# Kernel tuning notes

Measured on AMD Instinct MI355X. Metric: run time of the kernel, lower is better.

## Reference

```python
import jax, jax.numpy as jnp
import numpy as np


def setup_inputs() -> dict:
    key = jax.random.key(0)
    k1, k2 = jax.random.split(key)
    B, N, M = 8, 8192, 8192
    source_points = jax.random.normal(k1, (B, N, 3), dtype=jnp.float32)
    target_points = jax.random.normal(k2, (B, M, 3), dtype=jnp.float32)
    return {"source_points": source_points, "target_points": target_points}


def reference(source_points, target_points):
    # dist: [B, N, M]  (same math as (x[:, :, None] - y[:, None]) ** 2 summed over coords)
    s_sq = jnp.sum(source_points ** 2, axis=-1)  # [B, N]
    t_sq = jnp.sum(target_points ** 2, axis=-1)  # [B, M]
    cross = jnp.einsum("bnd,bmd->bnm", source_points, target_points)  # [B, N, M]
    dist = s_sq[:, :, None] + t_sq[:, None, :] - 2.0 * cross
    min_s2t = jnp.min(dist, axis=2)  # [B, N] nearest target for each source point
    min_t2s = jnp.min(dist, axis=1)  # [B, M] nearest source for each target point
    chamfer = jnp.mean(min_s2t, axis=1) + jnp.mean(min_t2s, axis=1)  # [B]
    return chamfer
```

## Files before the change

kernel.cpp:

```cpp
#include <hip/hip_runtime.h>


typedef float f32x16 __attribute__((ext_vector_type(16)));
typedef short bf16x8 __attribute__((ext_vector_type(8)));

constexpr int BATCH  = 8;
constexpr int NPTS   = 8192;
constexpr int BLOCK  = 256;
constexpr int QTILE  = 256;
constexpr int QB     = NPTS / QTILE;
constexpr int DSPLIT = 4;
constexpr int DBR    = NPTS / DSPLIT;
constexpr int CH     = 256;
constexpr int NCH    = DBR / CH;

constexpr size_t FRAGB_N = (size_t)BATCH * NPTS * 2;
constexpr size_t SM_N    = (size_t)BATCH * NPTS;

static __device__ __forceinline__ float fmin3(float a, float b, float c) {
    return fminf(fminf(a, b), c);
}
static __device__ __forceinline__ unsigned short bf16h(float f) {
    unsigned int u = __float_as_uint(f);
    u += 0x7fffu + ((u >> 16) & 1u);
    return (unsigned short)(u >> 16);
}
static __device__ __forceinline__ float bf16tof(unsigned short h) {
    return __uint_as_float(((unsigned int)h) << 16);
}
static __device__ __forceinline__ unsigned int pack2(unsigned short a, unsigned short b) {
    return (unsigned int)a | ((unsigned int)b << 16);
}
static __device__ __forceinline__ float tree16(const f32x16& a) {
    float m = fmin3(a[0], a[1], a[2]);
    m = fmin3(m, a[3], a[4]);   m = fmin3(m, a[5], a[6]);
    m = fmin3(m, a[7], a[8]);   m = fmin3(m, a[9], a[10]);
    m = fmin3(m, a[11], a[12]); m = fmin3(m, a[13], a[14]);
    return fminf(m, a[15]);
}

__global__ __launch_bounds__(BLOCK) void chamfer_prep(
    const float* __restrict__ tgt, uint4* __restrict__ fragB,
    unsigned int* __restrict__ smins, unsigned int* __restrict__ tmins,
    float* __restrict__ out)
{
    const int i = blockIdx.x * BLOCK + threadIdx.x;
    const float* tp = tgt + (size_t)i * 3;
    float px = tp[0], py = tp[1], pz = tp[2];
    float nx = -px, ny = -py, nz = -pz;
    float ht = 0.5f * fmaf(px, px, fmaf(py, py, pz * pz));
    const unsigned short one = bf16h(1.0f);
    unsigned short nxh = bf16h(nx), nxl = bf16h(nx - bf16tof(nxh));
    unsigned short nyh = bf16h(ny), nyl = bf16h(ny - bf16tof(nyh));
    unsigned short nzh = bf16h(nz), nzl = bf16h(nz - bf16tof(nzh));
    unsigned short hh = bf16h(ht),  hl = bf16h(ht - bf16tof(hh));
    fragB[2 * i + 0] = make_uint4(pack2(nxh, nxl), pack2(nxh, nyh),
                                  pack2(nyl, nyh), pack2(nzh, nzl));
    fragB[2 * i + 1] = make_uint4(pack2(nzh, one), pack2(one, hh),
                                  pack2(hl, 0), 0u);
    smins[i] = 0x7f7f7f7fu;
    tmins[i] = 0x7f7f7f7fu;
    if (i < BATCH) out[i] = 0.0f;
}

__global__ __launch_bounds__(BLOCK) void chamfer_nn(
    const float* __restrict__ src, const uint4* __restrict__ fragB,
    unsigned int* __restrict__ smins, unsigned int* __restrict__ tmins)
{
    __shared__ uint4 Bfr0[CH], Bfr1[CH];
    __shared__ int   sht[NCH][CH];

    const int tid  = threadIdx.x;
    const int lane = tid & 63;
    const int w    = tid >> 6;
    const int half = lane >> 5;
    const int l31  = lane & 31;
    const int qb   = blockIdx.x;
    const int b    = blockIdx.y;
    const int ds   = blockIdx.z;

#pragma unroll
    for (int c = 0; c < NCH; c++) sht[c][tid] = 0x7f7f7f7f;

    const unsigned short one = bf16h(1.0f);
    bf16x8 af0, af1;
#pragma unroll
    for (int g = 0; g < 2; g++) {
        const int q = qb * QTILE + w * 64 + g * 32 + l31;
        const float* qp = src + ((size_t)b * NPTS + q) * 3;
        float qx = qp[0], qy = qp[1], qz = qp[2];
        float hq = 0.5f * fmaf(qx, qx, fmaf(qy, qy, qz * qz));
        unsigned short xh = bf16h(qx), xl = bf16h(qx - bf16tof(xh));
        unsigned short yh = bf16h(qy), yl = bf16h(qy - bf16tof(yh));
        unsigned short zh = bf16h(qz), zl = bf16h(qz - bf16tof(zh));
        unsigned short qh = bf16h(hq), ql = bf16h(hq - bf16tof(qh));
        bf16x8 a;
        if (half == 0) {
            a[0] = (short)xh; a[1] = (short)xh; a[2] = (short)xl;
            a[3] = (short)yh; a[4] = (short)yh; a[5] = (short)yl;
            a[6] = (short)zh; a[7] = (short)zh;
        } else {
            a[0] = (short)zl; a[1] = (short)qh; a[2] = (short)ql;
            a[3] = (short)one; a[4] = (short)one;
            a[5] = 0; a[6] = 0; a[7] = 0;
        }
        if (g == 0) af0 = a; else af1 = a;
    }

    float rmn0[16], rmn1[16];
#pragma unroll
    for (int r = 0; r < 16; r++) { rmn0[r] = 3.4e38f; rmn1[r] = 3.4e38f; }
    const f32x16 zz = {};
    const uint4* Bh = half ? Bfr1 : Bfr0;

    const uint4* fb = fragB + ((size_t)b * NPTS + (size_t)ds * DBR) * 2;

    uint4 r0 = fb[2 * tid + 0], r1 = fb[2 * tid + 1];

    for (int c = 0; c < NCH; ++c) {
        __syncthreads();
        Bfr0[tid] = r0;
        Bfr1[tid] = r1;
        __syncthreads();
        if (c + 1 < NCH) {
            r0 = fb[2 * ((c + 1) * CH + tid) + 0];
            r1 = fb[2 * ((c + 1) * CH + tid) + 1];
        }

#pragma unroll
        for (int tp = 0; tp < CH / 64; ++tp) {
            const int t0 = tp * 2, t1 = tp * 2 + 1;
            bf16x8 b0 = *reinterpret_cast<const bf16x8*>(&Bh[t0 * 32 + l31]);
            bf16x8 b1 = *reinterpret_cast<const bf16x8*>(&Bh[t1 * 32 + l31]);
            f32x16 a00 = __builtin_amdgcn_mfma_f32_32x32x16_bf16(af0, b0, zz, 0, 0, 0);
            f32x16 a01 = __builtin_amdgcn_mfma_f32_32x32x16_bf16(af0, b1, zz, 0, 0, 0);
            f32x16 a10 = __builtin_amdgcn_mfma_f32_32x32x16_bf16(af1, b0, zz, 0, 0, 0);
            f32x16 a11 = __builtin_amdgcn_mfma_f32_32x32x16_bf16(af1, b1, zz, 0, 0, 0);
#pragma unroll
            for (int r = 0; r < 16; r++) {
                rmn0[r] = fmin3(rmn0[r], a00[r], a01[r]);
                rmn1[r] = fmin3(rmn1[r], a10[r], a11[r]);
            }
            float c0 = fminf(tree16(a00), tree16(a10));
            float c1 = fminf(tree16(a01), tree16(a11));
            atomicMin(&sht[c][t0 * 32 + l31], __float_as_int(c0));
            atomicMin(&sht[c][t1 * 32 + l31], __float_as_int(c1));
        }
    }
    __syncthreads();

    unsigned int* tm = tmins + (size_t)b * NPTS + (size_t)ds * DBR;
#pragma unroll
    for (int c = 0; c < NCH; c++) {
        float v = fmaxf(__int_as_float(sht[c][tid]), 0.0f);
        atomicMin(&tm[c * CH + tid], __float_as_uint(v));
    }

    unsigned int* sm = smins + (size_t)b * NPTS;
    const int qbase = qb * QTILE + w * 64;
#pragma unroll
    for (int r = 0; r < 16; r++) {
        float a = rmn0[r], bv = rmn1[r];
#pragma unroll
        for (int off = 16; off > 0; off >>= 1) {
            a  = fminf(a,  __shfl_xor(a,  off, 64));
            bv = fminf(bv, __shfl_xor(bv, off, 64));
        }
        if (l31 == 0) {
            const int row = (r & 3) + 8 * (r >> 2) + 4 * half;
            atomicMin(&sm[qbase + row],      __float_as_uint(fmaxf(a,  0.0f)));
            atomicMin(&sm[qbase + 32 + row], __float_as_uint(fmaxf(bv, 0.0f)));
        }
    }
}

__global__ __launch_bounds__(BLOCK) void chamfer_final(
    const unsigned int* __restrict__ smins, const unsigned int* __restrict__ tmins,
    float* __restrict__ out)
{
    const int seg = blockIdx.x;
    const int b   = blockIdx.y;
    const int tid = threadIdx.x;
    float acc = 0.0f;
#pragma unroll
    for (int k = 0; k < 8; k++) {
        const size_t i = (size_t)b * NPTS + seg * 2048 + k * BLOCK + tid;
        acc += __uint_as_float(smins[i]) + __uint_as_float(tmins[i]);
    }
    for (int off = 32; off > 0; off >>= 1) acc += __shfl_down(acc, off, 64);
    __shared__ float wsum[4];
    if ((tid & 63) == 0) wsum[tid >> 6] = acc;
    __syncthreads();
    if (tid == 0)
        atomicAdd(&out[b],
                  (wsum[0] + wsum[1] + wsum[2] + wsum[3]) * (2.0f / (float)NPTS));
}

extern "C" void kernel_launch(void* const* d_in, const int* in_sizes, int n_in,
                              void* d_out, int out_size, void* d_ws, size_t ws_size,
                              hipStream_t stream) {
    const float* src = (const float*)d_in[0];
    const float* tgt = (const float*)d_in[1];
    float* out = (float*)d_out;

    uint4* fragB        = (uint4*)d_ws;
    unsigned int* smins = (unsigned int*)(fragB + FRAGB_N);
    unsigned int* tmins = smins + SM_N;

    chamfer_prep<<<BATCH * NPTS / BLOCK, BLOCK, 0, stream>>>(tgt, fragB, smins, tmins, out);
    chamfer_nn<<<dim3(QB, BATCH, DSPLIT), BLOCK, 0, stream>>>(src, fragB, smins, tmins);
    chamfer_final<<<dim3(4, BATCH), BLOCK, 0, stream>>>(smins, tmins, out);
}
```

Before: 106.2 us.

## Compute both NN directions as separate row-min passes instead of column atomics

Drops the per-tile column reduction (tree16 plus LDS atomicMin per MFMA pair) that produced target-to-source minima. It adds a second set of blocks that swap the roles of source and target, so both directions use only the cheap row-min path, and it halves the database split to keep the grid size unchanged. This doubles the MFMA work in exchange for removing the heavy column-reduction ALU and LDS atomic traffic, and the prep kernel now builds fragments for both point sets.

```diff
diff --git a/kernel.cpp b/kernel.cpp
--- a/kernel.cpp
+++ b/kernel.cpp
@@ -9,13 +9,13 @@
 constexpr int BLOCK  = 256;
 constexpr int QTILE  = 256;
 constexpr int QB     = NPTS / QTILE;
-constexpr int DSPLIT = 4;
+constexpr int DSPLIT = 2;
 constexpr int DBR    = NPTS / DSPLIT;
 constexpr int CH     = 256;
 constexpr int NCH    = DBR / CH;
 
-constexpr size_t FRAGB_N = (size_t)BATCH * NPTS * 2;
-constexpr size_t SM_N    = (size_t)BATCH * NPTS;
+constexpr size_t FRAG_N = (size_t)BATCH * NPTS * 2;
+constexpr size_t SM_N   = (size_t)BATCH * NPTS;
 
 static __device__ __forceinline__ float fmin3(float a, float b, float c) {
     return fminf(fminf(a, b), c);
@@ -31,44 +31,48 @@
 static __device__ __forceinline__ unsigned int pack2(unsigned short a, unsigned short b) {
     return (unsigned int)a | ((unsigned int)b << 16);
 }
-static __device__ __forceinline__ float tree16(const f32x16& a) {
-    float m = fmin3(a[0], a[1], a[2]);
-    m = fmin3(m, a[3], a[4]);   m = fmin3(m, a[5], a[6]);
-    m = fmin3(m, a[7], a[8]);   m = fmin3(m, a[9], a[10]);
-    m = fmin3(m, a[11], a[12]); m = fmin3(m, a[13], a[14]);
-    return fminf(m, a[15]);
-}
-
-__global__ __launch_bounds__(BLOCK) void chamfer_prep(
-    const float* __restrict__ tgt, uint4* __restrict__ fragB,
-    unsigned int* __restrict__ smins, unsigned int* __restrict__ tmins,
-    float* __restrict__ out)
-{
-    const int i = blockIdx.x * BLOCK + threadIdx.x;
-    const float* tp = tgt + (size_t)i * 3;
-    float px = tp[0], py = tp[1], pz = tp[2];
+
+static __device__ __forceinline__ void make_bfrag(float px, float py, float pz,
+                                                  uint4& p0, uint4& p1) {
+    const unsigned short one = bf16h(1.0f);
     float nx = -px, ny = -py, nz = -pz;
     float ht = 0.5f * fmaf(px, px, fmaf(py, py, pz * pz));
-    const unsigned short one = bf16h(1.0f);
     unsigned short nxh = bf16h(nx), nxl = bf16h(nx - bf16tof(nxh));
     unsigned short nyh = bf16h(ny), nyl = bf16h(ny - bf16tof(nyh));
     unsigned short nzh = bf16h(nz), nzl = bf16h(nz - bf16tof(nzh));
     unsigned short hh = bf16h(ht),  hl = bf16h(ht - bf16tof(hh));
-    fragB[2 * i + 0] = make_uint4(pack2(nxh, nxl), pack2(nxh, nyh),
-                                  pack2(nyl, nyh), pack2(nzh, nzl));
-    fragB[2 * i + 1] = make_uint4(pack2(nzh, one), pack2(one, hh),
-                                  pack2(hl, 0), 0u);
-    smins[i] = 0x7f7f7f7fu;
-    tmins[i] = 0x7f7f7f7fu;
+    p0 = make_uint4(pack2(nxh, nxl), pack2(nxh, nyh),
+                    pack2(nyl, nyh), pack2(nzh, nzl));
+    p1 = make_uint4(pack2(nzh, one), pack2(one, hh),
+                    pack2(hl, 0), 0u);
+}
+
+__global__ __launch_bounds__(BLOCK) void chamfer_prep(
+    const float* __restrict__ src, const float* __restrict__ tgt,
+    uint4* __restrict__ fragS, uint4* __restrict__ fragT,
+    unsigned int* __restrict__ mins, float* __restrict__ out)
+{
+    const int i = blockIdx.x * BLOCK + threadIdx.x;
+    uint4 p0, p1;
+    const float* tp = tgt + (size_t)i * 3;
+    make_bfrag(tp[0], tp[1], tp[2], p0, p1);
+    fragT[2 * i + 0] = p0;
+    fragT[2 * i + 1] = p1;
+    const float* sp = src + (size_t)i * 3;
+    make_bfrag(sp[0], sp[1], sp[2], p0, p1);
+    fragS[2 * i + 0] = p0;
+    fragS[2 * i + 1] = p1;
+    mins[i]        = 0x7f7f7f7fu;
+    mins[SM_N + i] = 0x7f7f7f7fu;
     if (i < BATCH) out[i] = 0.0f;
 }
 
 __global__ __launch_bounds__(BLOCK) void chamfer_nn(
-    const float* __restrict__ src, const uint4* __restrict__ fragB,
-    unsigned int* __restrict__ smins, unsigned int* __restrict__ tmins)
+    const float* __restrict__ src, const float* __restrict__ tgt,
+    const uint4* __restrict__ fragS, const uint4* __restrict__ fragT,
+    unsigned int* __restrict__ mins)
 {
     __shared__ uint4 Bfr0[CH], Bfr1[CH];
-    __shared__ int   sht[NCH][CH];
 
     const int tid  = threadIdx.x;
     const int lane = tid & 63;
@@ -77,17 +81,18 @@
     const int l31  = lane & 31;
     const int qb   = blockIdx.x;
     const int b    = blockIdx.y;
-    const int ds   = blockIdx.z;
-
-#pragma unroll
-    for (int c = 0; c < NCH; c++) sht[c][tid] = 0x7f7f7f7f;
+    const int dir  = blockIdx.z / DSPLIT;
+    const int ds   = blockIdx.z % DSPLIT;
+
+    const float* P  = dir ? tgt : src;
+    const uint4* FB = dir ? fragS : fragT;
 
     const unsigned short one = bf16h(1.0f);
     bf16x8 af0, af1;
 #pragma unroll
     for (int g = 0; g < 2; g++) {
         const int q = qb * QTILE + w * 64 + g * 32 + l31;
-        const float* qp = src + ((size_t)b * NPTS + q) * 3;
+        const float* qp = P + ((size_t)b * NPTS + q) * 3;
         float qx = qp[0], qy = qp[1], qz = qp[2];
         float hq = 0.5f * fmaf(qx, qx, fmaf(qy, qy, qz * qz));
         unsigned short xh = bf16h(qx), xl = bf16h(qx - bf16tof(xh));
@@ -113,7 +118,7 @@
     const f32x16 zz = {};
     const uint4* Bh = half ? Bfr1 : Bfr0;
 
-    const uint4* fb = fragB + ((size_t)b * NPTS + (size_t)ds * DBR) * 2;
+    const uint4* fb = FB + ((size_t)b * NPTS + (size_t)ds * DBR) * 2;
 
     uint4 r0 = fb[2 * tid + 0], r1 = fb[2 * tid + 1];
 
@@ -141,22 +146,10 @@
                 rmn0[r] = fmin3(rmn0[r], a00[r], a01[r]);
                 rmn1[r] = fmin3(rmn1[r], a10[r], a11[r]);
             }
-            float c0 = fminf(tree16(a00), tree16(a10));
-            float c1 = fminf(tree16(a01), tree16(a11));
-            atomicMin(&sht[c][t0 * 32 + l31], __float_as_int(c0));
-            atomicMin(&sht[c][t1 * 32 + l31], __float_as_int(c1));
-        }
-    }
-    __syncthreads();
-
-    unsigned int* tm = tmins + (size_t)b * NPTS + (size_t)ds * DBR;
-#pragma unroll
-    for (int c = 0; c < NCH; c++) {
-        float v = fmaxf(__int_as_float(sht[c][tid]), 0.0f);
-        atomicMin(&tm[c * CH + tid], __float_as_uint(v));
-    }
-
-    unsigned int* sm = smins + (size_t)b * NPTS;
+        }
+    }
+
+    unsigned int* M = mins + ((size_t)dir * BATCH + b) * NPTS;
     const int qbase = qb * QTILE + w * 64;
 #pragma unroll
     for (int r = 0; r < 16; r++) {
@@ -168,15 +161,14 @@
         }
         if (l31 == 0) {
             const int row = (r & 3) + 8 * (r >> 2) + 4 * half;
-            atomicMin(&sm[qbase + row],      __float_as_uint(fmaxf(a,  0.0f)));
-            atomicMin(&sm[qbase + 32 + row], __float_as_uint(fmaxf(bv, 0.0f)));
+            atomicMin(&M[qbase + row],      __float_as_uint(fmaxf(a,  0.0f)));
+            atomicMin(&M[qbase + 32 + row], __float_as_uint(fmaxf(bv, 0.0f)));
         }
     }
 }
 
 __global__ __launch_bounds__(BLOCK) void chamfer_final(
-    const unsigned int* __restrict__ smins, const unsigned int* __restrict__ tmins,
-    float* __restrict__ out)
+    const unsigned int* __restrict__ mins, float* __restrict__ out)
 {
     const int seg = blockIdx.x;
     const int b   = blockIdx.y;
@@ -185,7 +177,7 @@
 #pragma unroll
     for (int k = 0; k < 8; k++) {
         const size_t i = (size_t)b * NPTS + seg * 2048 + k * BLOCK + tid;
-        acc += __uint_as_float(smins[i]) + __uint_as_float(tmins[i]);
+        acc += __uint_as_float(mins[i]) + __uint_as_float(mins[SM_N + i]);
     }
     for (int off = 32; off > 0; off >>= 1) acc += __shfl_down(acc, off, 64);
     __shared__ float wsum[4];
@@ -203,11 +195,13 @@
     const float* tgt = (const float*)d_in[1];
     float* out = (float*)d_out;
 
-    uint4* fragB        = (uint4*)d_ws;
-    unsigned int* smins = (unsigned int*)(fragB + FRAGB_N);
-    unsigned int* tmins = smins + SM_N;
-
-    chamfer_prep<<<BATCH * NPTS / BLOCK, BLOCK, 0, stream>>>(tgt, fragB, smins, tmins, out);
-    chamfer_nn<<<dim3(QB, BATCH, DSPLIT), BLOCK, 0, stream>>>(src, fragB, smins, tmins);
-    chamfer_final<<<dim3(4, BATCH), BLOCK, 0, stream>>>(smins, tmins, out);
-}
+    uint4* fragT        = (uint4*)d_ws;
+    uint4* fragS        = fragT + FRAG_N;
+    unsigned int* mins  = (unsigned int*)(fragS + FRAG_N);
+
+    chamfer_prep<<<BATCH * NPTS / BLOCK, BLOCK, 0, stream>>>(
+        src, tgt, fragS, fragT, mins, out);
+    chamfer_nn<<<dim3(QB, BATCH, 2 * DSPLIT), BLOCK, 0, stream>>>(
+        src, tgt, fragS, fragT, mins);
+    chamfer_final<<<dim3(4, BATCH), BLOCK, 0, stream>>>(mins, out);
+}
```

Result: slower. 111.8 us (+5.4%).
